# Optimization experiments

Hardware: AMD Instinct MI355X
Metric: run time of the kernel (lower is better)

## Reference

```python
import jax, jax.numpy as jnp
import numpy as np

SEARCH_RANGE = 4  # matches args.search_range


def _displacements(r):
    # Exact channel ordering of the original double loop:
    # I=0 -> (0,0); then for i=1..r: (-i,0),(+i,0),(0,-i),(0,+i),
    # then for j=1..r: (-i,-j),(+i,+j),(-i,+j),(+i,-j).
    ds = [(0, 0)]
    for i in range(1, r + 1):
        ds += [(-i, 0), (i, 0), (0, -i), (0, i)]
        for j in range(1, r + 1):
            ds += [(-i, -j), (i, j), (-i, j), (i, -j)]
    return ds


def setup_inputs() -> dict:
    key = jax.random.key(0)
    k1, k2 = jax.random.split(key)
    B, C, H, W = 4, 128, 96, 160
    src = jax.random.normal(k1, (B, C, H, W), dtype=jnp.float32)
    tgt = jax.random.normal(k2, (B, C, H, W), dtype=jnp.float32)
    return {"src": src, "tgt": tgt}


def reference(src, tgt):
    r = SEARCH_RANGE
    B, C, H, W = src.shape
    D = (2 * r + 1) ** 2  # 81 displacement channels
    # Zero-pad tgt spatially so out-of-range shifted regions contribute 0,
    # matching the torch version's zero-initialized output slices.
    tgt_pad = jnp.pad(tgt, ((0, 0), (0, 0), (r, r), (r, r)))
    chans = []
    for dy, dx in _displacements(r):
        # shifted[b,c,y,x] = tgt[b,c,y+dy,x+dx] (0 outside)
        t = jax.lax.dynamic_slice(tgt_pad, (0, 0, r + dy, r + dx), (B, C, H, W))
        chans.append(jnp.einsum('bchw,bchw->bhw', src, t))
    out = jnp.stack(chans, axis=1)  # [B, D, H, W]
    return out / D
```

## Files before the change

### kernel.cpp

```cpp
#include <hip/hip_runtime.h>
#include <hip/hip_bf16.h>

#define BATCH 4
#define CHAN 128
#define HGT 96
#define WID 160
#define HW (HGT * WID)
#define THREADS 256

typedef __attribute__((ext_vector_type(8))) short short8;
typedef __attribute__((ext_vector_type(4))) float float4v;

__device__ __forceinline__ int chan_of(int dy, int dx) {
    if (dy == 0 && dx == 0) return 0;
    if (dx == 0) { int i = dy < 0 ? -dy : dy; return 1 + (i - 1) * 20 + (dy < 0 ? 0 : 1); }
    if (dy == 0) { int i = dx < 0 ? -dx : dx; return 1 + (i - 1) * 20 + (dx < 0 ? 2 : 3); }
    int i = dy < 0 ? -dy : dy;
    int j = dx < 0 ? -dx : dx;
    int s = (dy < 0) ? (dx < 0 ? 0 : 2) : (dx < 0 ? 3 : 1);
    return 1 + (i - 1) * 20 + 4 + (j - 1) * 4 + s;
}

__device__ __forceinline__ unsigned pk2(float a, float b) {
    __hip_bfloat162 h = __float22bfloat162_rn(make_float2(a, b));
    unsigned u;
    __builtin_memcpy(&u, &h, 4);
    return u;
}

union sl_u { uint4 v; short8 s; };

__global__ __launch_bounds__(THREADS)
void cost_volume_kernel(const float* __restrict__ src,
                        const float* __restrict__ tgt,
                        float* __restrict__ out) {
    __shared__ __align__(16) uint4 s_b[2432];

    const int tid  = threadIdx.x;
    const int wv   = tid >> 6;
    const int lane = tid & 63;
    const int q    = lane >> 4;
    const int ln   = lane & 15;

    const int w    = blockIdx.x;
    const int slab = w & 7;
    const int b    = slab >> 1;
    const int yh   = slab & 1;
    const int r0   = w >> 3;
    const int dyg  = r0 % 3;
    const int t    = r0 / 3;
    const int x0   = (t % 10) * 16;
    const int y0   = yh * 48 + (t / 10) * 4;
    const int dy0  = dyg * 3 - 4;

    #pragma unroll
    for (int k = 0; k < 9; ++k) {
        const int u   = k * THREADS + tid;
        const int x   = u % 24;
        const int g   = u / 24;
        const int row = g % 6;
        const int oct = g / 6;
        const int gr  = y0 + dy0 + row;
        const int gx  = x0 - 4 + x;
        uint4 val = make_uint4(0u, 0u, 0u, 0u);
        if ((unsigned)gr < (unsigned)HGT && (unsigned)gx < (unsigned)WID) {
            const int off = ((b * CHAN + oct * 8) * HGT + gr) * WID + gx;
            float v0 = tgt[off];
            float v1 = tgt[off + 1 * HW];
            float v2 = tgt[off + 2 * HW];
            float v3 = tgt[off + 3 * HW];
            float v4 = tgt[off + 4 * HW];
            float v5 = tgt[off + 5 * HW];
            float v6 = tgt[off + 6 * HW];
            float v7 = tgt[off + 7 * HW];
            val.x = pk2(v0, v1);
            val.y = pk2(v2, v3);
            val.z = pk2(v4, v5);
            val.w = pk2(v6, v7);
        }
        s_b[(row * 24 + x) * 16 + (oct ^ (x & 15))] = val;
    }

    const int y  = y0 + wv;
    const int sb = (b * CHAN * HGT + y) * WID + x0 + ln + q * 8 * HW;
    short8 afr[4];
    #pragma unroll
    for (int ks = 0; ks < 4; ++ks) {
        float av[8];
        #pragma unroll
        for (int j = 0; j < 8; ++j)
            av[j] = src[sb + (ks * 32 + j) * HW];
        sl_u f;
        f.v.x = pk2(av[0], av[1]);
        f.v.y = pk2(av[2], av[3]);
        f.v.z = pk2(av[4], av[5]);
        f.v.w = pk2(av[6], av[7]);
        afr[ks] = f.s;
    }

    __syncthreads();

    const float inv = 1.0f / 81.0f;
    #pragma unroll
    for (int dyi = 0; dyi < 3; ++dyi) {
        const int dy = dy0 + dyi;
        const int rr = wv + dyi;
        float4v a0 = (float4v){0.f, 0.f, 0.f, 0.f};
        float4v a1 = (float4v){0.f, 0.f, 0.f, 0.f};
        #pragma unroll
        for (int ks = 0; ks < 4; ++ks) {
            sl_u b0;
            b0.v = s_b[(rr * 24 + ln) * 16 + ((q + ks * 4) ^ ln)];
            a0 = __builtin_amdgcn_mfma_f32_16x16x32_bf16(afr[ks], b0.s, a0, 0, 0, 0);
        }
        #pragma unroll
        for (int ks = 0; ks < 4; ++ks) {
            sl_u b1;
            b1.v = s_b[(rr * 24 + 16 + ln) * 16 + ((q + ks * 4) ^ ln)];
            a1 = __builtin_amdgcn_mfma_f32_16x16x32_bf16(afr[ks], b1.s, a1, 0, 0, 0);
        }
        #pragma unroll
        for (int reg = 0; reg < 4; ++reg) {
            const int m = q * 4 + reg;
            {
                int dx = ln - 4 - m;
                if (dx >= -4 && dx <= 4) {
                    int oc = chan_of(dy, dx);
                    out[((b * 81 + oc) * HGT + y) * WID + x0 + m] = a0[reg] * inv;
                }
            }
            {
                int dx = 16 + ln - 4 - m;
                if (dx >= -4 && dx <= 4) {
                    int oc = chan_of(dy, dx);
                    out[((b * 81 + oc) * HGT + y) * WID + x0 + m] = a1[reg] * inv;
                }
            }
        }
    }
}

extern "C" void kernel_launch(void* const* d_in, const int* in_sizes, int n_in,
                              void* d_out, int out_size, void* d_ws, size_t ws_size,
                              hipStream_t stream) {
    const float* src = (const float*)d_in[0];
    const float* tgt = (const float*)d_in[1];
    float* out = (float*)d_out;
    cost_volume_kernel<<<dim3(2880, 1, 1), dim3(THREADS, 1, 1), 0, stream>>>(src, tgt, out);
}
```

Measured before the change: 128.8 us.

## Vectorize tgt staging loads, batch global loads early, table-drive output channels

Replaces the scalar per-element tgt staging loop with float4 vector loads covering four x positions per thread, issued in three batches interleaved with the src fragment loads so more memory requests are in flight before the bf16 packing and LDS writes. Output channel offsets are precomputed into a small shared table instead of evaluating chan_of per store. Launch bounds now request 4 blocks per CU, which limits registers despite the larger live load buffers. The float4 loads assume 16-byte alignment of x0-4, which holds because x0 is a multiple of 16.

```diff
diff --git a/kernel.cpp b/kernel.cpp
--- a/kernel.cpp
+++ b/kernel.cpp
@@ -30,11 +30,41 @@
 
 union sl_u { uint4 v; short8 s; };
 
-__global__ __launch_bounds__(THREADS)
+#define ST_DECODE(TAG, U)                                                     \
+    const int oct##TAG = (U) & 15;                                            \
+    const int u4##TAG  = (U) >> 4;                                            \
+    const int row##TAG = (u4##TAG * 43) >> 8;        \
+    const int xq##TAG  = u4##TAG - row##TAG * 6;                              \
+    const int gr##TAG  = y0 + dy0 + row##TAG;                                 \
+    const int gx##TAG  = x0 - 4 + xq##TAG * 4;               \
+    const bool ok##TAG = ((unsigned)gr##TAG < (unsigned)HGT) &&               \
+                         ((unsigned)gx##TAG < (unsigned)WID);                 \
+    const int ga##TAG  = tb + (oct##TAG * 8 * HGT + gr##TAG) * WID + gx##TAG;
+
+#define ST_ISSUE(TAG, COND)                                                   \
+    _Pragma("unroll")                                                         \
+    for (int j = 0; j < 8; ++j)                                               \
+        p##TAG[j] = (COND) ? *(const float4v*)(tgt + ga##TAG + j * HW)        \
+                           : (float4v){0.f, 0.f, 0.f, 0.f};
+
+#define ST_WRITE(TAG)                                                         \
+    _Pragma("unroll")                                                         \
+    for (int i = 0; i < 4; ++i) {                                             \
+        const int xl = xq##TAG * 4 + i;                                       \
+        uint4 val;                                                            \
+        val.x = pk2(p##TAG[0][i], p##TAG[1][i]);                              \
+        val.y = pk2(p##TAG[2][i], p##TAG[3][i]);                              \
+        val.z = pk2(p##TAG[4][i], p##TAG[5][i]);                              \
+        val.w = pk2(p##TAG[6][i], p##TAG[7][i]);                              \
+        s_b[(row##TAG * 24 + xl) * 16 + (oct##TAG ^ (xl & 15))] = val;        \
+    }
+
+__global__ __launch_bounds__(THREADS, 4)
 void cost_volume_kernel(const float* __restrict__ src,
                         const float* __restrict__ tgt,
                         float* __restrict__ out) {
     __shared__ __align__(16) uint4 s_b[2432];
+    __shared__ int s_tab[27];
 
     const int tid  = threadIdx.x;
     const int wv   = tid >> 6;
@@ -53,57 +83,51 @@
     const int y0   = yh * 48 + (t / 10) * 4;
     const int dy0  = dyg * 3 - 4;
 
-    #pragma unroll
-    for (int k = 0; k < 9; ++k) {
-        const int u   = k * THREADS + tid;
-        const int x   = u % 24;
-        const int g   = u / 24;
-        const int row = g % 6;
-        const int oct = g / 6;
-        const int gr  = y0 + dy0 + row;
-        const int gx  = x0 - 4 + x;
-        uint4 val = make_uint4(0u, 0u, 0u, 0u);
-        if ((unsigned)gr < (unsigned)HGT && (unsigned)gx < (unsigned)WID) {
-            const int off = ((b * CHAN + oct * 8) * HGT + gr) * WID + gx;
-            float v0 = tgt[off];
-            float v1 = tgt[off + 1 * HW];
-            float v2 = tgt[off + 2 * HW];
-            float v3 = tgt[off + 3 * HW];
-            float v4 = tgt[off + 4 * HW];
-            float v5 = tgt[off + 5 * HW];
-            float v6 = tgt[off + 6 * HW];
-            float v7 = tgt[off + 7 * HW];
-            val.x = pk2(v0, v1);
-            val.y = pk2(v2, v3);
-            val.z = pk2(v4, v5);
-            val.w = pk2(v6, v7);
-        }
-        s_b[(row * 24 + x) * 16 + (oct ^ (x & 15))] = val;
-    }
+    if (tid < 27) s_tab[tid] = chan_of(dy0 + tid / 9, tid % 9 - 4) * HW;
+
+    const int tb = b * CHAN * HGT * WID;
+
+    ST_DECODE(0, tid)
+    ST_DECODE(1, tid + 256)
+    ST_DECODE(2, tid + 512)
+    const bool has2 = tid < 64;
+
+    float4v p0[8], p1[8], p2[8];
+
+    ST_ISSUE(0, ok0)
 
     const int y  = y0 + wv;
-    const int sb = (b * CHAN * HGT + y) * WID + x0 + ln + q * 8 * HW;
+    const int sbase = (b * CHAN * HGT + y) * WID + x0 + ln + q * 8 * HW;
+    float apay[32];
+    #pragma unroll
+    for (int ks = 0; ks < 4; ++ks)
+        #pragma unroll
+        for (int j = 0; j < 8; ++j)
+            apay[ks * 8 + j] = src[sbase + (ks * 32 + j) * HW];
+
+    ST_ISSUE(1, ok1)
+
+    ST_WRITE(0)
+    ST_ISSUE(2, has2 && ok2)
     short8 afr[4];
     #pragma unroll
     for (int ks = 0; ks < 4; ++ks) {
-        float av[8];
-        #pragma unroll
-        for (int j = 0; j < 8; ++j)
-            av[j] = src[sb + (ks * 32 + j) * HW];
         sl_u f;
-        f.v.x = pk2(av[0], av[1]);
-        f.v.y = pk2(av[2], av[3]);
-        f.v.z = pk2(av[4], av[5]);
-        f.v.w = pk2(av[6], av[7]);
+        f.v.x = pk2(apay[ks * 8 + 0], apay[ks * 8 + 1]);
+        f.v.y = pk2(apay[ks * 8 + 2], apay[ks * 8 + 3]);
+        f.v.z = pk2(apay[ks * 8 + 4], apay[ks * 8 + 5]);
+        f.v.w = pk2(apay[ks * 8 + 6], apay[ks * 8 + 7]);
         afr[ks] = f.s;
     }
+    ST_WRITE(1)
+    if (has2) { ST_WRITE(2) }
 
     __syncthreads();
 
     const float inv = 1.0f / 81.0f;
+    const int obase = (b * 81 * HGT + y) * WID + x0;
     #pragma unroll
     for (int dyi = 0; dyi < 3; ++dyi) {
-        const int dy = dy0 + dyi;
         const int rr = wv + dyi;
         float4v a0 = (float4v){0.f, 0.f, 0.f, 0.f};
         float4v a1 = (float4v){0.f, 0.f, 0.f, 0.f};
@@ -122,20 +146,12 @@
         #pragma unroll
         for (int reg = 0; reg < 4; ++reg) {
             const int m = q * 4 + reg;
-            {
-                int dx = ln - 4 - m;
-                if (dx >= -4 && dx <= 4) {
-                    int oc = chan_of(dy, dx);
-                    out[((b * 81 + oc) * HGT + y) * WID + x0 + m] = a0[reg] * inv;
-                }
-            }
-            {
-                int dx = 16 + ln - 4 - m;
-                if (dx >= -4 && dx <= 4) {
-                    int oc = chan_of(dy, dx);
-                    out[((b * 81 + oc) * HGT + y) * WID + x0 + m] = a1[reg] * inv;
-                }
-            }
+            const int t0x = ln - m;
+            if ((unsigned)t0x <= 8u)
+                out[obase + s_tab[dyi * 9 + t0x] + m] = a0[reg] * inv;
+            const int t1x = ln + 16 - m;
+            if ((unsigned)t1x <= 8u)
+                out[obase + s_tab[dyi * 9 + t1x] + m] = a1[reg] * inv;
         }
     }
 }
```

Result: slower. 136.6 us (+6.1%).
